# Optimization experiments

Measured on AMD Instinct MI355X. Metric: run time of the kernel, lower is better.

Reference implementation:

```python
import jax, jax.numpy as jnp
import numpy as np

L = 65536
D = 256

def setup_inputs() -> dict:
    key = jax.random.key(0)
    k1, k2, k3 = jax.random.split(key, 3)
    K = jax.random.normal(k1, (L, D), dtype=jnp.float32)
    V = jax.random.normal(k2, (L, D), dtype=jnp.float32)
    q = jax.random.normal(k3, (D,), dtype=jnp.float32)  # nn.Parameter(torch.randn(d_model))
    return {"K": K, "V": V, "q": q, "mode": 0}

def reference(K, V, q, mode):
    # s[i] = <K[i], q>; online-softmax recurrence over the sequence dim.
    s = K @ q  # [L]
    neg_inf = jnp.float32(-jnp.inf)

    def step(carry, inp):
        m_prev, u_prev, w_prev = carry
        s_i, v_i = inp
        m = jnp.maximum(m_prev, s_i)
        e_prev = jnp.exp(m_prev - m)
        e_curr = jnp.exp(s_i - m)
        u = u_prev * e_prev + e_curr
        w = w_prev * e_prev + v_i * e_curr  # [D]
        return (m, u, w), w / u

    init = (neg_inf, jnp.float32(0.0), jnp.zeros((D,), dtype=V.dtype))
    _, out = jax.lax.scan(step, init, (s, V))  # out: [L, D]
    return out
```

## Files before the change

kernel.cpp:

```cpp
#include <hip/hip_runtime.h>
#include <math.h>

#define L_TOTAL 65536
#define D_DIM   256
#define C_ROWS  32
#define N_CHUNK (L_TOTAL / C_ROWS)
#define SUPER   32
#define N_SUPER (N_CHUNK / SUPER)

__global__ __launch_bounds__(256) void kA_aggregate(
    const float* __restrict__ K, const float* __restrict__ V,
    const float* __restrict__ q,
    float* __restrict__ s_g, float* __restrict__ cm,
    float* __restrict__ cu, float* __restrict__ cw)
{
    const int t = threadIdx.x;
    const int c = blockIdx.x;
    const int r0 = c * C_ROWS;
    const int wave = t >> 6, lane = t & 63;

    __shared__ float s_lds[C_ROWS];
    __shared__ float red[C_ROWS];
    __shared__ float coef[C_ROWS];

    const float4 q4 = *reinterpret_cast<const float4*>(q + 4 * lane);

    float4 kv[8];
    #pragma unroll
    for (int k = 0; k < 8; ++k) {
        const int row = r0 + wave * 8 + k;
        kv[k] = *reinterpret_cast<const float4*>(K + (size_t)row * D_DIM + 4 * lane);
    }
    #pragma unroll
    for (int k = 0; k < 8; ++k) {
        float d = kv[k].x * q4.x + kv[k].y * q4.y + kv[k].z * q4.z + kv[k].w * q4.w;
        #pragma unroll
        for (int off = 32; off > 0; off >>= 1) d += __shfl_xor(d, off, 64);
        if (lane == 0) s_lds[wave * 8 + k] = d;
    }
    __syncthreads();

    if (t < C_ROWS) { s_g[r0 + t] = s_lds[t]; red[t] = s_lds[t]; }
    __syncthreads();
    for (int off = 16; off > 0; off >>= 1) {
        if (t < off) red[t] = fmaxf(red[t], red[t + off]);
        __syncthreads();
    }
    const float m_c = red[0];
    __syncthreads();
    if (t < C_ROWS) { coef[t] = __expf(s_lds[t] - m_c); red[t] = coef[t]; }
    __syncthreads();
    for (int off = 16; off > 0; off >>= 1) {
        if (t < off) red[t] += red[t + off];
        __syncthreads();
    }
    const float u_c = red[0];

    float w = 0.f;
    const float* Vp = V + (size_t)r0 * D_DIM + t;
    #pragma unroll 8
    for (int j = 0; j < C_ROWS; ++j)
        w = fmaf(coef[j], Vp[(size_t)j * D_DIM], w);

    cw[(size_t)c * D_DIM + t] = w;
    if (t == 0) { cm[c] = m_c; cu[c] = u_c; }
}

__global__ __launch_bounds__(256) void kB_scalar_scan(
    const float* __restrict__ cm, const float* __restrict__ cu,
    float* __restrict__ pm, float* __restrict__ pu)
{
    const int t = threadIdx.x;
    __shared__ float Lm[256], Lu[256];

    float am[8], au[8];
    float M = -INFINITY, U = 0.f;
    #pragma unroll
    for (int j = 0; j < 8; ++j) {
        am[j] = cm[8 * t + j]; au[j] = cu[8 * t + j];
        const float mm = fmaxf(M, am[j]);
        U = U * __expf(M - mm) + au[j] * __expf(am[j] - mm);
        M = mm;
    }
    Lm[t] = M; Lu[t] = U;
    float Mi = M, Ui = U;
    __syncthreads();
    for (int off = 1; off < 256; off <<= 1) {
        float m1 = 0.f, u1 = 0.f;
        const bool act = (t >= off);
        if (act) { m1 = Lm[t - off]; u1 = Lu[t - off]; }
        __syncthreads();
        if (act) {
            const float mm = fmaxf(m1, Mi);
            Ui = u1 * __expf(m1 - mm) + Ui * __expf(Mi - mm);
            Mi = mm;
            Lm[t] = Mi; Lu[t] = Ui;
        }
        __syncthreads();
    }
    float Me = (t == 0) ? -INFINITY : Lm[t - 1];
    float Ue = (t == 0) ? 0.f : Lu[t - 1];
    #pragma unroll
    for (int j = 0; j < 8; ++j) {
        pm[8 * t + j] = Me; pu[8 * t + j] = Ue;
        const float mm = fmaxf(Me, am[j]);
        Ue = Ue * __expf(Me - mm) + au[j] * __expf(am[j] - mm);
        Me = mm;
    }
    if (t == 255) { pm[N_CHUNK] = Me; pu[N_CHUNK] = Ue; }
}

__global__ __launch_bounds__(256) void kC_super_scan(
    const float* __restrict__ cm, const float* __restrict__ cw,
    const float* __restrict__ pm,
    float* __restrict__ pwl, float* __restrict__ T)
{
    const int t = threadIdx.x;
    const int S = blockIdx.x;
    __shared__ float ca[SUPER], cb[SUPER];

    if (t < SUPER) {
        const int c = S * SUPER + t;
        ca[t] = __expf(pm[c] - pm[c + 1]);
        cb[t] = __expf(cm[c] - pm[c + 1]);
    }
    __syncthreads();

    float PW = 0.f;
    #pragma unroll 4
    for (int j = 0; j < SUPER; ++j) {
        const int c = S * SUPER + j;
        pwl[(size_t)c * D_DIM + t] = PW;
        const float wv = cw[(size_t)c * D_DIM + t];
        PW = PW * ca[j] + wv * cb[j];
    }
    T[(size_t)S * D_DIM + t] = PW;
}

__global__ __launch_bounds__(256) void kD_top_scan(
    const float* __restrict__ pm, const float* __restrict__ T,
    float* __restrict__ sw)
{
    const int t = threadIdx.x;
    float SW = 0.f;
    for (int S = 0; S < N_SUPER; ++S) {
        sw[(size_t)S * D_DIM + t] = SW;
        const float g = __expf(pm[S * SUPER] - pm[(S + 1) * SUPER]);
        SW = SW * g + T[(size_t)S * D_DIM + t];
    }
}

__global__ __launch_bounds__(256) void kF_output(
    const float* __restrict__ V, const float* __restrict__ s_g,
    const float* __restrict__ pm, const float* __restrict__ pu,
    const float* __restrict__ pwl, const float* __restrict__ sw,
    float* __restrict__ out)
{
    const int t = threadIdx.x;
    const int c = blockIdx.x;
    const int S = c / SUPER;
    const int r0 = c * C_ROWS;

    __shared__ float sm[C_ROWS], su[C_ROWS];
    __shared__ float sa[C_ROWS], se[C_ROWS], sri[C_ROWS];

    float sv = 0.f;
    if (t < C_ROWS) {
        sv = s_g[r0 + t];
        sm[t] = sv; su[t] = 1.f;
    }
    float m = sv, u = 1.f;
    __syncthreads();
    for (int off = 1; off < C_ROWS; off <<= 1) {
        float m1 = 0.f, u1 = 0.f;
        const bool act = (t >= off) && (t < C_ROWS);
        if (act) { m1 = sm[t - off]; u1 = su[t - off]; }
        __syncthreads();
        if (act) {
            const float mm = fmaxf(m1, m);
            u = u1 * __expf(m1 - mm) + u * __expf(m - mm);
            m = mm;
            sm[t] = m; su[t] = u;
        }
        __syncthreads();
    }
    const float pmc = pm[c];
    if (t < C_ROWS) {
        const float puc = pu[c];
        const float mrow = fmaxf(pmc, m);
        const float urow = puc * __expf(pmc - mrow) + u * __expf(m - mrow);
        const float mprev = (t == 0) ? pmc : fmaxf(pmc, sm[t - 1]);
        sa[t]  = __expf(mprev - mrow);
        se[t]  = __expf(sv - mrow);
        sri[t] = 1.0f / urow;
    }
    __syncthreads();

    const float g = (c == 0) ? 0.f : __expf(pm[S * SUPER] - pmc);
    float W = sw[(size_t)S * D_DIM + t] * g + pwl[(size_t)c * D_DIM + t];

    const float* Vp = V + (size_t)r0 * D_DIM + t;
    float* Op = out + (size_t)r0 * D_DIM + t;
    #pragma unroll 8
    for (int j = 0; j < C_ROWS; ++j) {
        const float v = Vp[(size_t)j * D_DIM];
        W = W * sa[j] + v * se[j];
        Op[(size_t)j * D_DIM] = W * sri[j];
    }
}

extern "C" void kernel_launch(void* const* d_in, const int* in_sizes, int n_in,
                              void* d_out, int out_size, void* d_ws, size_t ws_size,
                              hipStream_t stream) {
    const float* K = (const float*)d_in[0];
    const float* V = (const float*)d_in[1];
    const float* q = (const float*)d_in[2];
    float* out = (float*)d_out;

    float* ws  = (float*)d_ws;
    float* s_g = ws;
    float* cm  = s_g + L_TOTAL;
    float* cu  = cm + N_CHUNK;
    float* pm  = cu + N_CHUNK;
    float* pu  = pm + (N_CHUNK + 16);
    float* cw  = pu + (N_CHUNK + 16);
    float* pwl = cw + (size_t)N_CHUNK * D_DIM;
    float* T   = pwl + (size_t)N_CHUNK * D_DIM;
    float* sw  = T + (size_t)N_SUPER * D_DIM;

    kA_aggregate<<<N_CHUNK, 256, 0, stream>>>(K, V, q, s_g, cm, cu, cw);
    kB_scalar_scan<<<1, 256, 0, stream>>>(cm, cu, pm, pu);
    kC_super_scan<<<N_SUPER, 256, 0, stream>>>(cm, cw, pm, pwl, T);
    kD_top_scan<<<1, 256, 0, stream>>>(pm, T, sw);
    kF_output<<<N_CHUNK, 256, 0, stream>>>(V, s_g, pm, pu, pwl, sw, out);
}
```

Baseline: 202.1 us.

## Prefetch V and cw into registers, replace LDS scans with per-thread reductions and wave shuffles

Each kernel now issues all of its global loads (V rows, cw rows, T rows) into register arrays up front, so memory latency overlaps with the dot-product and scan work. The barrier-heavy LDS tree reductions in the aggregate kernel become redundant per-thread loops over shared scores. The output kernel's LDS Hillis-Steele scan becomes a single-wave shuffle scan. The top scan precomputes its exp factors in shared memory, at the cost of higher register pressure and possibly lower occupancy.

```diff
diff --git a/kernel.cpp b/kernel.cpp
--- a/kernel.cpp
+++ b/kernel.cpp
@@ -20,17 +20,19 @@
     const int wave = t >> 6, lane = t & 63;
 
     __shared__ float s_lds[C_ROWS];
-    __shared__ float red[C_ROWS];
-    __shared__ float coef[C_ROWS];
+
+    float v[C_ROWS];
+    const float* Vp = V + (size_t)r0 * D_DIM + t;
+    #pragma unroll
+    for (int j = 0; j < C_ROWS; ++j) v[j] = Vp[(size_t)j * D_DIM];
 
     const float4 q4 = *reinterpret_cast<const float4*>(q + 4 * lane);
-
+    const float* Kp = K + (size_t)(r0 + wave * 8) * D_DIM + 4 * lane;
     float4 kv[8];
     #pragma unroll
-    for (int k = 0; k < 8; ++k) {
-        const int row = r0 + wave * 8 + k;
-        kv[k] = *reinterpret_cast<const float4*>(K + (size_t)row * D_DIM + 4 * lane);
-    }
+    for (int k = 0; k < 8; ++k)
+        kv[k] = *reinterpret_cast<const float4*>(Kp + (size_t)k * D_DIM);
+
     #pragma unroll
     for (int k = 0; k < 8; ++k) {
         float d = kv[k].x * q4.x + kv[k].y * q4.y + kv[k].z * q4.z + kv[k].w * q4.w;
@@ -40,27 +42,19 @@
     }
     __syncthreads();
 
-    if (t < C_ROWS) { s_g[r0 + t] = s_lds[t]; red[t] = s_lds[t]; }
-    __syncthreads();
-    for (int off = 16; off > 0; off >>= 1) {
-        if (t < off) red[t] = fmaxf(red[t], red[t + off]);
-        __syncthreads();
-    }
-    const float m_c = red[0];
-    __syncthreads();
-    if (t < C_ROWS) { coef[t] = __expf(s_lds[t] - m_c); red[t] = coef[t]; }
-    __syncthreads();
-    for (int off = 16; off > 0; off >>= 1) {
-        if (t < off) red[t] += red[t + off];
-        __syncthreads();
-    }
-    const float u_c = red[0];
-
-    float w = 0.f;
-    const float* Vp = V + (size_t)r0 * D_DIM + t;
-    #pragma unroll 8
-    for (int j = 0; j < C_ROWS; ++j)
-        w = fmaf(coef[j], Vp[(size_t)j * D_DIM], w);
+    if (t < C_ROWS) s_g[r0 + t] = s_lds[t];
+
+    float m_c = -INFINITY;
+    #pragma unroll
+    for (int j = 0; j < C_ROWS; ++j) m_c = fmaxf(m_c, s_lds[j]);
+
+    float u_c = 0.f, w = 0.f;
+    #pragma unroll
+    for (int j = 0; j < C_ROWS; ++j) {
+        const float cf = __expf(s_lds[j] - m_c);
+        u_c += cf;
+        w = fmaf(cf, v[j], w);
+    }
 
     cw[(size_t)c * D_DIM + t] = w;
     if (t == 0) { cm[c] = m_c; cu[c] = u_c; }
@@ -119,6 +113,11 @@
     const int S = blockIdx.x;
     __shared__ float ca[SUPER], cb[SUPER];
 
+    float wv[SUPER];
+    const float* cwp = cw + (size_t)S * SUPER * D_DIM + t;
+    #pragma unroll
+    for (int j = 0; j < SUPER; ++j) wv[j] = cwp[(size_t)j * D_DIM];
+
     if (t < SUPER) {
         const int c = S * SUPER + t;
         ca[t] = __expf(pm[c] - pm[c + 1]);
@@ -127,12 +126,11 @@
     __syncthreads();
 
     float PW = 0.f;
-    #pragma unroll 4
+    float* pwlp = pwl + (size_t)S * SUPER * D_DIM + t;
+    #pragma unroll
     for (int j = 0; j < SUPER; ++j) {
-        const int c = S * SUPER + j;
-        pwl[(size_t)c * D_DIM + t] = PW;
-        const float wv = cw[(size_t)c * D_DIM + t];
-        PW = PW * ca[j] + wv * cb[j];
+        pwlp[(size_t)j * D_DIM] = PW;
+        PW = PW * ca[j] + wv[j] * cb[j];
     }
     T[(size_t)S * D_DIM + t] = PW;
 }
@@ -142,11 +140,21 @@
     float* __restrict__ sw)
 {
     const int t = threadIdx.x;
+    __shared__ float g[N_SUPER];
+
+    float tv[N_SUPER];
+    #pragma unroll
+    for (int S = 0; S < N_SUPER; ++S) tv[S] = T[(size_t)S * D_DIM + t];
+
+    if (t < N_SUPER)
+        g[t] = __expf(pm[t * SUPER] - pm[(t + 1) * SUPER]);
+    __syncthreads();
+
     float SW = 0.f;
+    #pragma unroll
     for (int S = 0; S < N_SUPER; ++S) {
         sw[(size_t)S * D_DIM + t] = SW;
-        const float g = __expf(pm[S * SUPER] - pm[(S + 1) * SUPER]);
-        SW = SW * g + T[(size_t)S * D_DIM + t];
+        SW = SW * g[S] + tv[S];
     }
 }
 
@@ -160,51 +168,54 @@
     const int c = blockIdx.x;
     const int S = c / SUPER;
     const int r0 = c * C_ROWS;
-
-    __shared__ float sm[C_ROWS], su[C_ROWS];
+    const int wave = t >> 6, lane = t & 63;
+
     __shared__ float sa[C_ROWS], se[C_ROWS], sri[C_ROWS];
 
-    float sv = 0.f;
-    if (t < C_ROWS) {
-        sv = s_g[r0 + t];
-        sm[t] = sv; su[t] = 1.f;
-    }
-    float m = sv, u = 1.f;
-    __syncthreads();
-    for (int off = 1; off < C_ROWS; off <<= 1) {
-        float m1 = 0.f, u1 = 0.f;
-        const bool act = (t >= off) && (t < C_ROWS);
-        if (act) { m1 = sm[t - off]; u1 = su[t - off]; }
-        __syncthreads();
-        if (act) {
-            const float mm = fmaxf(m1, m);
-            u = u1 * __expf(m1 - mm) + u * __expf(m - mm);
-            m = mm;
-            sm[t] = m; su[t] = u;
+    float v[C_ROWS];
+    const float* Vp = V + (size_t)r0 * D_DIM + t;
+    #pragma unroll
+    for (int j = 0; j < C_ROWS; ++j) v[j] = Vp[(size_t)j * D_DIM];
+
+    const float seed_pwl = pwl[(size_t)c * D_DIM + t];
+    const float seed_sw  = sw[(size_t)S * D_DIM + t];
+    const float pmc = pm[c];
+    const float pmS = pm[S * SUPER];
+
+    if (wave == 0) {
+        const float puc = pu[c];
+        float s_val = -INFINITY;
+        if (lane < C_ROWS) s_val = s_g[r0 + lane];
+        float m = s_val, u = 1.0f;
+        #pragma unroll
+        for (int off = 1; off < C_ROWS; off <<= 1) {
+            const float m1 = __shfl_up(m, off, 32);
+            const float u1 = __shfl_up(u, off, 32);
+            if ((lane & 31) >= off) {
+                const float mm = fmaxf(m1, m);
+                u = u1 * __expf(m1 - mm) + u * __expf(m - mm);
+                m = mm;
+            }
         }
-        __syncthreads();
-    }
-    const float pmc = pm[c];
-    if (t < C_ROWS) {
-        const float puc = pu[c];
-        const float mrow = fmaxf(pmc, m);
-        const float urow = puc * __expf(pmc - mrow) + u * __expf(m - mrow);
-        const float mprev = (t == 0) ? pmc : fmaxf(pmc, sm[t - 1]);
-        sa[t]  = __expf(mprev - mrow);
-        se[t]  = __expf(sv - mrow);
-        sri[t] = 1.0f / urow;
-    }
-    __syncthreads();
-
-    const float g = (c == 0) ? 0.f : __expf(pm[S * SUPER] - pmc);
-    float W = sw[(size_t)S * D_DIM + t] * g + pwl[(size_t)c * D_DIM + t];
-
-    const float* Vp = V + (size_t)r0 * D_DIM + t;
+        const float m_row = fmaxf(pmc, m);
+        const float u_row = puc * __expf(pmc - m_row) + u * __expf(m - m_row);
+        const float m_prev_raw = __shfl_up(m_row, 1, 32);
+        const float m_prev = ((lane & 31) == 0) ? pmc : m_prev_raw;
+        if (lane < C_ROWS) {
+            sa[lane]  = __expf(m_prev - m_row);
+            se[lane]  = __expf(s_val - m_row);
+            sri[lane] = 1.0f / u_row;
+        }
+    }
+    __syncthreads();
+
+    const float gf = (c == 0) ? 0.f : __expf(pmS - pmc);
+    float W = seed_sw * gf + seed_pwl;
+
     float* Op = out + (size_t)r0 * D_DIM + t;
-    #pragma unroll 8
+    #pragma unroll
     for (int j = 0; j < C_ROWS; ++j) {
-        const float v = Vp[(size_t)j * D_DIM];
-        W = W * sa[j] + v * se[j];
+        W = W * sa[j] + v[j] * se[j];
         Op[(size_t)j * D_DIM] = W * sri[j];
     }
 }
```

Result: faster. 194.6 us (-3.7%).
